# Kernel tuning notes

Hardware: AMD Instinct MI355X
Metric: run time of the kernel (lower is better)

## Reference

```python
import jax, jax.numpy as jnp
import numpy as np

N = 50000      # nodes
E = 800000     # edges (avg degree 16)
F_IN = 128     # num_features
H = 64         # hidden_dim
G = 64         # graphs in batch


def setup_inputs() -> dict:
    key = jax.random.key(0)
    ks = jax.random.split(key, 20)
    inp = {
        "x": jax.random.normal(ks[0], (N, F_IN), jnp.float32),
        "edge_index": jax.random.randint(ks[1], (2, E), 0, N, dtype=jnp.int32).astype(jnp.int64),
        "batch": jnp.sort(jax.random.randint(ks[2], (N,), 0, G, dtype=jnp.int32)).astype(jnp.int64),
    }
    # GraphConv layer dims: in -> out
    dims = [(F_IN, H), (H, 2 * H), (2 * H, 3 * H), (3 * H, H)]
    k = 3
    for i, (din, dout) in enumerate(dims):
        s = 1.0 / np.sqrt(din).astype(np.float32)
        inp[f"w{i+1}_rel"] = jax.random.normal(ks[k], (din, dout), jnp.float32) * s
        inp[f"w{i+1}_root"] = jax.random.normal(ks[k + 1], (din, dout), jnp.float32) * s
        inp[f"b{i+1}"] = jnp.zeros((dout,), jnp.float32)
        k += 2
    inp["head_w"] = jax.random.normal(ks[k], (H, 1), jnp.float32) * (1.0 / np.sqrt(H).astype(np.float32))
    inp["head_b"] = jnp.zeros((1,), jnp.float32)
    return inp


def _graph_conv(x, src, dst, w_rel, w_root, b):
    # PyG GraphConv: out = lin_rel(sum_{j in N(i)} x_j) + lin_root(x_i)
    agg = jax.ops.segment_sum(x[src], dst, num_segments=N)  # [N, din]
    return agg @ w_rel + b + x @ w_root


def reference(x, edge_index, batch,
              w1_rel, w1_root, b1,
              w2_rel, w2_root, b2,
              w3_rel, w3_root, b3,
              w4_rel, w4_root, b4,
              head_w, head_b):
    src, dst = edge_index[0], edge_index[1]
    h = jax.nn.relu(_graph_conv(x, src, dst, w1_rel, w1_root, b1))
    h = jax.nn.relu(_graph_conv(h, src, dst, w2_rel, w2_root, b2))
    h = jax.nn.relu(_graph_conv(h, src, dst, w3_rel, w3_root, b3))
    h = _graph_conv(h, src, dst, w4_rel, w4_root, b4)          # [N, H]
    # global_mean_pool over graph ids
    sums = jax.ops.segment_sum(h, batch, num_segments=G)       # [G, H]
    counts = jax.ops.segment_sum(jnp.ones((N,), h.dtype), batch, num_segments=G)
    pooled = sums / jnp.maximum(counts, 1.0)[:, None]          # [G, H]
    return pooled @ head_w + head_b                            # [G, 1]
```

## Files before the change

kernel.cpp:

```cpp
#include <hip/hip_runtime.h>


#define NNODES 50000
#define NEDGES 800000
#define NGRAPH 64
#define NBUK 256
#define BSZ 196
#define EPB (NEDGES / NBUK)
#define CVT_NB (NNODES * 128 / 4 / 256)
#define PACK_NB (160 * 512 / 256)
#define PREP_NB (CVT_NB + PACK_NB + 1)
#define RGRID ((NNODES + 127) / 128)
#define RCHUNK ((RGRID + 7) / 8)

typedef __attribute__((ext_vector_type(8))) __bf16 bf16x8;
typedef __attribute__((ext_vector_type(16))) float f32x16;

__device__ __forceinline__ unsigned short f2bf(float f) {
    unsigned u = __float_as_uint(f);
    u += 0x7fff + ((u >> 16) & 1);
    return (unsigned short)(u >> 16);
}
__device__ __forceinline__ float bf2f(unsigned b) {
    return __uint_as_float(b << 16);
}

__device__ __forceinline__ void dma16(const void* g, void* l) {
    __builtin_amdgcn_global_load_lds(
        (const __attribute__((address_space(1))) void*)g,
        (__attribute__((address_space(3))) void*)l, 16, 0, 0);
}


__device__ __forceinline__ void pack32(const float* __restrict__ W, unsigned short* __restrict__ dst,
                                       int KS_tot, int ks0, int dcols, int ct0,
                                       int tl, int ksl, int lane, int j) {
    int k = ksl * 16 + ((lane >> 5) << 3) + j;
    int col = tl * 32 + (lane & 31);
    dst[(((size_t)(ct0 + tl) * KS_tot + (ks0 + ksl)) * 64 + lane) * 8 + j] = f2bf(W[k * dcols + col]);
}

__device__ void prep_body(int b, int tid,
                          const float* x, unsigned short* xbf,
                          const float* w1_rel, const float* w1_root,
                          const float* w2_rel, const float* w2_root,
                          const float* w3_rel, const float* w3_root,
                          unsigned short* pL1, unsigned short* pL2, unsigned short* pL3,
                          const float* w4_rel, const float* w4_root,
                          const float* b4, const float* head_w,
                          float* wr, float* wt, float* cbuf) {
    if (b < CVT_NB) {
        int i = b * 256 + tid;
        float4 v = ((const float4*)x)[i];
        unsigned lo = (unsigned)f2bf(v.x) | ((unsigned)f2bf(v.y) << 16);
        unsigned hi = (unsigned)f2bf(v.z) | ((unsigned)f2bf(v.w) << 16);
        ((uint2*)xbf)[i] = make_uint2(lo, hi);
    } else if (b < CVT_NB + PACK_NB) {
        int idx = (b - CVT_NB) * 256 + tid;
        int g = idx >> 9;
        int t = idx & 511;
        int lane = (t >> 3) & 63, j = t & 7;
        if (g < 16)       { int gl = g;       pack32(w1_rel,  pL1, 8,  0, 64,  0, gl / 8, gl % 8, lane, j); }
        else if (g < 32)  { int gl = g - 16;  pack32(w1_root, pL1, 8,  0, 64,  2, gl / 8, gl % 8, lane, j); }
        else if (g < 48)  { int gl = g - 32;  pack32(w2_rel,  pL2, 8,  0, 128, 0, gl / 4, gl % 4, lane, j); }
        else if (g < 64)  { int gl = g - 48;  pack32(w2_root, pL2, 8,  4, 128, 0, gl / 4, gl % 4, lane, j); }
        else if (g < 112) { int gl = g - 64;  pack32(w3_rel,  pL3, 16, 0, 192, 0, gl / 8, gl % 8, lane, j); }
        else              { int gl = g - 112; pack32(w3_root, pL3, 16, 8, 192, 0, gl / 8, gl % 8, lane, j); }
    } else {
        if (tid < 192) {
            float ar = 0.f, at = 0.f;
            for (int j = 0; j < 64; j++) {
                float hw = head_w[j];
                ar = fmaf(w4_rel[tid * 64 + j], hw, ar);
                at = fmaf(w4_root[tid * 64 + j], hw, at);
            }
            wr[tid] = ar;
            wt[tid] = at;
        } else if (tid == 192) {
            float c = 0.f;
            for (int j = 0; j < 64; j++) c = fmaf(b4[j], head_w[j], c);
            cbuf[0] = c;
        }
    }
}


__global__ void __launch_bounds__(256) histprep_kernel(
    const int* __restrict__ edst, int* __restrict__ bcnt,
    const float* __restrict__ x, unsigned short* __restrict__ xbf,
    const float* __restrict__ w1_rel, const float* __restrict__ w1_root,
    const float* __restrict__ w2_rel, const float* __restrict__ w2_root,
    const float* __restrict__ w3_rel, const float* __restrict__ w3_root,
    unsigned short* __restrict__ pL1, unsigned short* __restrict__ pL2,
    unsigned short* __restrict__ pL3,
    const float* __restrict__ w4_rel, const float* __restrict__ w4_root,
    const float* __restrict__ b4, const float* __restrict__ head_w,
    float* __restrict__ wr, float* __restrict__ wt, float* __restrict__ cbuf)
{
    int tid = threadIdx.x, b = blockIdx.x;
    if (b < NBUK) {
        __shared__ int h[NBUK];
        h[tid] = 0;
        __syncthreads();
        int end = (b + 1) * EPB;
        for (int i = b * EPB + tid; i < end; i += 256)
            atomicAdd(&h[edst[i] / BSZ], 1);
        __syncthreads();
        bcnt[tid * NBUK + b] = h[tid];
    } else {
        prep_body(b - NBUK, tid, x, xbf, w1_rel, w1_root, w2_rel, w2_root,
                  w3_rel, w3_root, pL1, pL2, pL3, w4_rel, w4_root, b4, head_w,
                  wr, wt, cbuf);
    }
}


__global__ void scan1_kernel(int* __restrict__ a, int* __restrict__ bsum, int n) {
    __shared__ int buf[256];
    int tid = threadIdx.x;
    int i = blockIdx.x * 256 + tid;
    int v = (i < n) ? a[i] : 0;
    buf[tid] = v;
    __syncthreads();
    #pragma unroll
    for (int off = 1; off < 256; off <<= 1) {
        int t = (tid >= off) ? buf[tid - off] : 0;
        __syncthreads();
        buf[tid] += t;
        __syncthreads();
    }
    if (i < n) a[i] = buf[tid] - v;
    if (tid == 255) bsum[blockIdx.x] = buf[255];
}

__global__ void scan2_kernel(int* __restrict__ bsum, int nb) {
    __shared__ int buf[256];
    int tid = threadIdx.x;
    int v = (tid < nb) ? bsum[tid] : 0;
    buf[tid] = v;
    __syncthreads();
    #pragma unroll
    for (int off = 1; off < 256; off <<= 1) {
        int t = (tid >= off) ? buf[tid - off] : 0;
        __syncthreads();
        buf[tid] += t;
        __syncthreads();
    }
    if (tid < nb) bsum[tid] = buf[tid] - v;
}

__global__ void partition_kernel(const int* __restrict__ src, const int* __restrict__ dst,
                                 const int* __restrict__ cnt, const int* __restrict__ bsum,
                                 unsigned long long* __restrict__ pedge) {
    __shared__ int lbase[NBUK];
    int tid = threadIdx.x, k = blockIdx.x;
    lbase[tid] = cnt[tid * NBUK + k] + bsum[tid];
    __syncthreads();
    int end = (k + 1) * EPB;
    for (int i = k * EPB + tid; i < end; i += 256) {
        int s = src[i], d = dst[i];
        int pos = atomicAdd(&lbase[d / BSZ], 1);
        pedge[pos] = (unsigned long long)(unsigned)s | ((unsigned long long)(unsigned)d << 32);
    }
}

__global__ void build_kernel(const unsigned long long* __restrict__ pedge,
                             const int* __restrict__ bsum,
                             int* __restrict__ rp, int* __restrict__ csr) {
    __shared__ int sdeg[256], sc[256], sbase[256], sfill[256];
    int tid = threadIdx.x, b = blockIdx.x;
    int node0 = b * BSZ;
    int ncnt = NNODES - node0;
    if (ncnt > BSZ) ncnt = BSZ;
    if (ncnt < 0) ncnt = 0;
    int seg0 = bsum[b];
    int seg1 = (b + 1 < NBUK) ? bsum[b + 1] : NEDGES;
    sdeg[tid] = 0;
    sfill[tid] = 0;
    __syncthreads();
    for (int i = seg0 + tid; i < seg1; i += 256)
        atomicAdd(&sdeg[(int)(pedge[i] >> 32) - node0], 1);
    __syncthreads();
    sc[tid] = sdeg[tid];
    __syncthreads();
    #pragma unroll
    for (int off = 1; off < 256; off <<= 1) {
        int t = (tid >= off) ? sc[tid - off] : 0;
        __syncthreads();
        sc[tid] += t;
        __syncthreads();
    }
    sbase[tid] = sc[tid] - sdeg[tid];
    if (tid < ncnt) rp[node0 + tid] = seg0 + sbase[tid];
    if (b == NBUK - 1 && tid == 0) rp[NNODES] = NEDGES;
    __syncthreads();
    for (int i = seg0 + tid; i < seg1; i += 256) {
        unsigned long long p = pedge[i];
        int d = (int)(p >> 32) - node0;
        int pos = atomicAdd(&sfill[d], 1);
        csr[seg0 + sbase[d] + pos] = (int)(p & 0xffffffffu);
    }
}


template<int KS, int NT, int NHALF, int ST, int KCH>
__global__ __launch_bounds__(256) void gemm_v5(
    const unsigned short* __restrict__ A, const unsigned short* __restrict__ Wall,
    const float* __restrict__ bias, unsigned short* __restrict__ OUT,
    int ldo, int ocol0, int relu, int N,
    const float* __restrict__ wrp, const float* __restrict__ wtp,
    float* __restrict__ sb, float* __restrict__ tb)
{
    const int K = KS * 16;
    const int CPC = KCH * 2;
    __shared__ __align__(16) unsigned short sB[NT * KS * 512];
    __shared__ __align__(16) unsigned short sA[128 * KCH * 16];

    int i = blockIdx.x;
    int chunk = i / (8 * NHALF);
    int rem = i - chunk * (8 * NHALF);
    int halfsel = rem >> 3;
    int rowb = chunk * 8 + (rem & 7);
    int rbase = rowb * 128;
    if (rbase >= N) return;

    int tid = threadIdx.x;
    int wave = tid >> 6, lane = tid & 63;
    int l32 = lane & 31, half = lane >> 5;
    const unsigned short* W = Wall + (size_t)halfsel * NT * KS * 512;

    #pragma unroll
    for (int j = 0; j < NT * KS * 64 / 256; j++) {
        int p = j * 256 + wave * 64;
        dma16(W + ((size_t)p + lane) * 8, sB + (size_t)p * 8);
    }

    f32x16 acc[NT];
    #pragma unroll
    for (int t = 0; t < NT; t++)
        #pragma unroll
        for (int r = 0; r < 16; r++) acc[t][r] = 0.f;

    int lr = wave * 32 + l32;

    for (int kb = 0; kb < KS; kb += KCH) {
        if (kb > 0) __syncthreads();
        #pragma unroll
        for (int j = 0; j < 128 * CPC / 256; j++) {
            int p = j * 256 + wave * 64 + lane;
            int r = p / CPC;
            int c = p - r * CPC;
            int cg = c ^ (r & (CPC - 1));
            dma16(A + (size_t)(rbase + r) * K + kb * 16 + cg * 8,
                  sA + (size_t)(j * 256 + wave * 64) * 8);
        }
        __syncthreads();
        #pragma unroll
        for (int l = 0; l < KCH; l++) {
            int cs = (l * 2 + half) ^ (lr & (CPC - 1));
            bf16x8 a = *(const bf16x8*)(sA + (size_t)lr * (KCH * 16) + cs * 8);
            int ks = kb + l;
            #pragma unroll
            for (int t = 0; t < NT; t++) {
                bf16x8 b = *(const bf16x8*)(sB + ((size_t)(t * KS + ks) * 64 + lane) * 8);
                acc[t] = __builtin_amdgcn_mfma_f32_32x32x16_bf16(a, b, acc[t], 0, 0, 0);
            }
        }
    }

    int wrbase = rbase + wave * 32;
    if constexpr (ST) {
        #pragma unroll
        for (int reg = 0; reg < 16; reg++) {
            int row = wrbase + (reg & 3) + 8 * (reg >> 2) + 4 * half;
            float sv = 0.f, tv = 0.f;
            #pragma unroll
            for (int t = 0; t < NT; t++) {
                int col = halfsel * NT * 32 + t * 32 + l32;
                float v = fmaxf(acc[t][reg] + bias[col], 0.f);
                sv = fmaf(v, wrp[col], sv);
                tv = fmaf(v, wtp[col], tv);
            }
            #pragma unroll
            for (int m = 1; m < 32; m <<= 1) {
                sv += __shfl_xor(sv, m, 64);
                tv += __shfl_xor(tv, m, 64);
            }
            if (l32 == 0 && row < N) {
                atomicAdd(&sb[row], sv);
                atomicAdd(&tb[row], tv);
            }
        }
    } else {
        #pragma unroll
        for (int t = 0; t < NT; t++) {
            int col = t * 32 + l32;
            float bi = bias ? bias[col] : 0.f;
            #pragma unroll
            for (int reg = 0; reg < 16; reg++) {
                int row = wrbase + (reg & 3) + 8 * (reg >> 2) + 4 * half;
                if (row < N) {
                    float v = acc[t][reg] + bi;
                    if (relu) v = fmaxf(v, 0.f);
                    OUT[(size_t)row * ldo + ocol0 + col] = f2bf(v);
                }
            }
        }
    }
}


__device__ __forceinline__ void acc8(float* a, uint4 u) {
    a[0] += bf2f(u.x & 0xffffu); a[1] += bf2f(u.x >> 16);
    a[2] += bf2f(u.y & 0xffffu); a[3] += bf2f(u.y >> 16);
    a[4] += bf2f(u.z & 0xffffu); a[5] += bf2f(u.z >> 16);
    a[6] += bf2f(u.w & 0xffffu); a[7] += bf2f(u.w >> 16);
}

template<int LPF, int SUBS>
__global__ void agg_kernel_v4(const unsigned short* __restrict__ X, int ldx,
                              const int* __restrict__ rp, const int* __restrict__ csr,
                              const unsigned short* __restrict__ root, int ldr,
                              const float* __restrict__ bias, int relu,
                              unsigned short* __restrict__ OUT, int ldo, int N) {
    int t = blockIdx.x * blockDim.x + threadIdx.x;
    int node = t / (SUBS * LPF);
    int r = t % (SUBS * LPF);
    int sub = r / LPF;
    int sl = r % LPF;
    if (node >= N) return;
    float a[8] = {0.f, 0.f, 0.f, 0.f, 0.f, 0.f, 0.f, 0.f};
    int e0 = rp[node], e1 = rp[node + 1];
    const unsigned short* xb = X + 8 * sl;
    int e = e0 + sub;
    for (; e + 3 * SUBS < e1; e += 4 * SUBS) {
        int s0 = csr[e], s1 = csr[e + SUBS], s2 = csr[e + 2 * SUBS], s3 = csr[e + 3 * SUBS];
        uint4 u0 = *(const uint4*)(xb + (size_t)s0 * ldx);
        uint4 u1 = *(const uint4*)(xb + (size_t)s1 * ldx);
        uint4 u2 = *(const uint4*)(xb + (size_t)s2 * ldx);
        uint4 u3 = *(const uint4*)(xb + (size_t)s3 * ldx);
        acc8(a, u0); acc8(a, u1); acc8(a, u2); acc8(a, u3);
    }
    for (; e < e1; e += SUBS) {
        uint4 u = *(const uint4*)(xb + (size_t)csr[e] * ldx);
        acc8(a, u);
    }
    #pragma unroll
    for (int m = LPF; m < SUBS * LPF; m <<= 1)
        #pragma unroll
        for (int i = 0; i < 8; i++) a[i] += __shfl_xor(a[i], m, 64);
    if (sub == 0) {
        if (root) {
            uint4 u = *(const uint4*)(root + (size_t)node * ldr + 8 * sl);
            acc8(a, u);
        }
        if (bias) {
            float4 b0 = *(const float4*)(bias + 8 * sl);
            float4 b1 = *(const float4*)(bias + 8 * sl + 4);
            a[0] += b0.x; a[1] += b0.y; a[2] += b0.z; a[3] += b0.w;
            a[4] += b1.x; a[5] += b1.y; a[6] += b1.z; a[7] += b1.w;
        }
        if (relu) {
            #pragma unroll
            for (int i = 0; i < 8; i++) a[i] = fmaxf(a[i], 0.f);
        }
        uint4 o;
        o.x = (unsigned)f2bf(a[0]) | ((unsigned)f2bf(a[1]) << 16);
        o.y = (unsigned)f2bf(a[2]) | ((unsigned)f2bf(a[3]) << 16);
        o.z = (unsigned)f2bf(a[4]) | ((unsigned)f2bf(a[5]) << 16);
        o.w = (unsigned)f2bf(a[6]) | ((unsigned)f2bf(a[7]) << 16);
        *(uint4*)(OUT + (size_t)node * ldo + 8 * sl) = o;
    }
}


__global__ void aggpool_kernel(const float* __restrict__ s, const float* __restrict__ t,
                               const int* __restrict__ rp, const int* __restrict__ csr,
                               const int* __restrict__ batch, float* __restrict__ gsum,
                               int* __restrict__ cnt, int N) {
    __shared__ float ls[NGRAPH];
    __shared__ int lc[NGRAPH];
    int tid = threadIdx.x;
    if (tid < NGRAPH) { ls[tid] = 0.f; lc[tid] = 0; }
    __syncthreads();
    int n = blockIdx.x * blockDim.x + tid;
    if (n < N) {
        float a = 0.f;
        int e = rp[n], e1 = rp[n + 1];
        for (; e + 3 < e1; e += 4) {
            int s0 = csr[e], s1 = csr[e + 1], s2 = csr[e + 2], s3 = csr[e + 3];
            a += s[s0] + s[s1] + s[s2] + s[s3];
        }
        for (; e < e1; e++) a += s[csr[e]];
        int g = batch[n];
        atomicAdd(&ls[g], a + t[n]);
        atomicAdd(&lc[g], 1);
    }
    __syncthreads();
    if (tid < NGRAPH && lc[tid] > 0) {
        atomicAdd(&gsum[tid], ls[tid]);
        atomicAdd(&cnt[tid], lc[tid]);
    }
}

__global__ void final_kernel(const float* __restrict__ gsum, const int* __restrict__ cnt,
                             const float* __restrict__ cbuf, const float* __restrict__ head_b,
                             float* __restrict__ out) {
    int g = threadIdx.x;
    if (g < NGRAPH) {
        float c = (float)(cnt[g] > 0 ? cnt[g] : 1);
        out[g] = gsum[g] / c + cbuf[0] + head_b[0];
    }
}


extern "C" void kernel_launch(void* const* d_in, const int* in_sizes, int n_in,
                              void* d_out, int out_size, void* d_ws, size_t ws_size,
                              hipStream_t stream) {
    const float* x       = (const float*)d_in[0];
    const int*   edge    = (const int*)d_in[1];
    const int*   batch   = (const int*)d_in[2];
    const float* w1_rel  = (const float*)d_in[3];
    const float* w1_root = (const float*)d_in[4];
    const float* b1      = (const float*)d_in[5];
    const float* w2_rel  = (const float*)d_in[6];
    const float* w2_root = (const float*)d_in[7];
    const float* b2      = (const float*)d_in[8];
    const float* w3_rel  = (const float*)d_in[9];
    const float* w3_root = (const float*)d_in[10];
    const float* b3      = (const float*)d_in[11];
    const float* w4_rel  = (const float*)d_in[12];
    const float* w4_root = (const float*)d_in[13];
    const float* b4      = (const float*)d_in[14];
    const float* head_w  = (const float*)d_in[15];
    const float* head_b  = (const float*)d_in[16];
    float* out = (float*)d_out;

    const int N = NNODES, E = NEDGES;
    const int* esrc = edge;
    const int* edst = edge + E;

    char* ws = (char*)d_ws;
    size_t off = 0;
    auto alloc = [&](size_t bytes) -> char* {
        char* p = ws + off;
        off = (off + bytes + 255) & ~(size_t)255;
        return p;
    };
    float* gsum  = (float*)alloc(NGRAPH * 4);
    int*   cnt   = (int*)alloc(NGRAPH * 4);
    float* sbuf  = (float*)alloc((size_t)N * 4);
    float* tbuf  = (float*)alloc((size_t)N * 4);
    size_t zero_bytes = off;
    int*   bcnt  = (int*)alloc((size_t)NBUK * NBUK * 4);
    int*   bsum  = (int*)alloc(256 * 4);
    int*   rp    = (int*)alloc((size_t)(N + 1) * 4);
    int*   csr   = (int*)alloc((size_t)E * 4);
    unsigned long long* pedge = (unsigned long long*)alloc((size_t)E * 8);
    unsigned short* xbf    = (unsigned short*)alloc((size_t)N * 128 * 2);
    unsigned short* z1     = (unsigned short*)alloc((size_t)N * 128 * 2);
    unsigned short* combo2 = (unsigned short*)alloc((size_t)N * 128 * 2);
    unsigned short* combo3 = (unsigned short*)alloc((size_t)N * 256 * 2);
    unsigned short* pL1    = (unsigned short*)alloc(4 * 8 * 512 * 2);
    unsigned short* pL2    = (unsigned short*)alloc(4 * 8 * 512 * 2);
    unsigned short* pL3    = (unsigned short*)alloc(6 * 16 * 512 * 2);
    float* wr    = (float*)alloc(192 * 4);
    float* wt    = (float*)alloc(192 * 4);
    float* cbuf  = (float*)alloc(4);
    (void)ws_size;

    hipMemsetAsync(gsum, 0, zero_bytes, stream);

    const int TB = 256;

    histprep_kernel<<<NBUK + PREP_NB, 256, 0, stream>>>(
        edst, bcnt, x, xbf, w1_rel, w1_root, w2_rel, w2_root, w3_rel, w3_root,
        pL1, pL2, pL3, w4_rel, w4_root, b4, head_w, wr, wt, cbuf);
    scan1_kernel<<<NBUK, 256, 0, stream>>>(bcnt, bsum, NBUK * NBUK);
    scan2_kernel<<<1, 256, 0, stream>>>(bsum, NBUK);
    partition_kernel<<<NBUK, 256, 0, stream>>>(esrc, edst, bcnt, bsum, pedge);
    build_kernel<<<NBUK, 256, 0, stream>>>(pedge, bsum, rp, csr);

    gemm_v5<8, 4, 1, 0, 8><<<RCHUNK * 8, 256, 0, stream>>>(
        xbf, pL1, nullptr, z1, 128, 0, 0, N, nullptr, nullptr, nullptr, nullptr);
    agg_kernel_v4<8, 2><<<(N * 16 + TB - 1) / TB, TB, 0, stream>>>(z1, 128, rp, csr,
                                                                   z1 + 64, 128, b1, 1, combo2 + 64, 128, N);
    agg_kernel_v4<8, 2><<<(N * 16 + TB - 1) / TB, TB, 0, stream>>>(combo2 + 64, 128, rp, csr,
                                                                   nullptr, 0, nullptr, 0, combo2, 128, N);
    gemm_v5<8, 4, 1, 0, 8><<<RCHUNK * 8, 256, 0, stream>>>(
        combo2, pL2, b2, combo3, 256, 128, 1, N, nullptr, nullptr, nullptr, nullptr);
    agg_kernel_v4<16, 2><<<(N * 32 + TB - 1) / TB, TB, 0, stream>>>(combo3 + 128, 256, rp, csr,
                                                                    nullptr, 0, nullptr, 0, combo3, 256, N);
    gemm_v5<16, 3, 2, 1, 4><<<RCHUNK * 8 * 2, 256, 0, stream>>>(
        combo3, pL3, b3, nullptr, 0, 0, 0, N, wr, wt, sbuf, tbuf);

    aggpool_kernel<<<(N + TB - 1) / TB, TB, 0, stream>>>(sbuf, tbuf, rp, csr, batch, gsum, cnt, N);
    final_kernel<<<1, 64, 0, stream>>>(gsum, cnt, cbuf, head_b, out);
}
```

Measured before the change: 245.5 us.

## Fuse CSR-build stages with first GEMM and fold scans and memset into kernels

Merges the second-level scan into each partition block, which re-scans the bucket sums redundantly. The layer-1 GEMM blocks are split across the partition and build kernels so the independent GEMM work overlaps with the CSR construction. The memset is folded into the scan kernel as extra zeroing blocks. Three kernel launches are removed, at the cost of 64KB of shared memory per block in the fused kernels, which may reduce occupancy for the partition and build blocks.

```diff
diff --git a/kernel.cpp b/kernel.cpp
--- a/kernel.cpp
+++ b/kernel.cpp
@@ -12,6 +12,8 @@
 #define PREP_NB (CVT_NB + PACK_NB + 1)
 #define RGRID ((NNODES + 127) / 128)
 #define RCHUNK ((RGRID + 7) / 8)
+#define GB_SPLIT 196
+#define ZNB 32
 
 typedef __attribute__((ext_vector_type(8))) __bf16 bf16x8;
 typedef __attribute__((ext_vector_type(16))) float f32x16;
@@ -115,96 +117,34 @@
 }
 
 
-__global__ void scan1_kernel(int* __restrict__ a, int* __restrict__ bsum, int n) {
+__global__ void scanzero_kernel(int* __restrict__ a, int* __restrict__ bsum, int n,
+                                float4* __restrict__ zb, int zn16) {
     __shared__ int buf[256];
-    int tid = threadIdx.x;
-    int i = blockIdx.x * 256 + tid;
-    int v = (i < n) ? a[i] : 0;
-    buf[tid] = v;
-    __syncthreads();
-    #pragma unroll
-    for (int off = 1; off < 256; off <<= 1) {
-        int t = (tid >= off) ? buf[tid - off] : 0;
-        __syncthreads();
-        buf[tid] += t;
-        __syncthreads();
-    }
-    if (i < n) a[i] = buf[tid] - v;
-    if (tid == 255) bsum[blockIdx.x] = buf[255];
-}
-
-__global__ void scan2_kernel(int* __restrict__ bsum, int nb) {
-    __shared__ int buf[256];
-    int tid = threadIdx.x;
-    int v = (tid < nb) ? bsum[tid] : 0;
-    buf[tid] = v;
-    __syncthreads();
-    #pragma unroll
-    for (int off = 1; off < 256; off <<= 1) {
-        int t = (tid >= off) ? buf[tid - off] : 0;
-        __syncthreads();
-        buf[tid] += t;
-        __syncthreads();
-    }
-    if (tid < nb) bsum[tid] = buf[tid] - v;
-}
-
-__global__ void partition_kernel(const int* __restrict__ src, const int* __restrict__ dst,
-                                 const int* __restrict__ cnt, const int* __restrict__ bsum,
-                                 unsigned long long* __restrict__ pedge) {
-    __shared__ int lbase[NBUK];
-    int tid = threadIdx.x, k = blockIdx.x;
-    lbase[tid] = cnt[tid * NBUK + k] + bsum[tid];
-    __syncthreads();
-    int end = (k + 1) * EPB;
-    for (int i = k * EPB + tid; i < end; i += 256) {
-        int s = src[i], d = dst[i];
-        int pos = atomicAdd(&lbase[d / BSZ], 1);
-        pedge[pos] = (unsigned long long)(unsigned)s | ((unsigned long long)(unsigned)d << 32);
-    }
-}
-
-__global__ void build_kernel(const unsigned long long* __restrict__ pedge,
-                             const int* __restrict__ bsum,
-                             int* __restrict__ rp, int* __restrict__ csr) {
-    __shared__ int sdeg[256], sc[256], sbase[256], sfill[256];
     int tid = threadIdx.x, b = blockIdx.x;
-    int node0 = b * BSZ;
-    int ncnt = NNODES - node0;
-    if (ncnt > BSZ) ncnt = BSZ;
-    if (ncnt < 0) ncnt = 0;
-    int seg0 = bsum[b];
-    int seg1 = (b + 1 < NBUK) ? bsum[b + 1] : NEDGES;
-    sdeg[tid] = 0;
-    sfill[tid] = 0;
-    __syncthreads();
-    for (int i = seg0 + tid; i < seg1; i += 256)
-        atomicAdd(&sdeg[(int)(pedge[i] >> 32) - node0], 1);
-    __syncthreads();
-    sc[tid] = sdeg[tid];
-    __syncthreads();
-    #pragma unroll
-    for (int off = 1; off < 256; off <<= 1) {
-        int t = (tid >= off) ? sc[tid - off] : 0;
-        __syncthreads();
-        sc[tid] += t;
-        __syncthreads();
-    }
-    sbase[tid] = sc[tid] - sdeg[tid];
-    if (tid < ncnt) rp[node0 + tid] = seg0 + sbase[tid];
-    if (b == NBUK - 1 && tid == 0) rp[NNODES] = NEDGES;
-    __syncthreads();
-    for (int i = seg0 + tid; i < seg1; i += 256) {
-        unsigned long long p = pedge[i];
-        int d = (int)(p >> 32) - node0;
-        int pos = atomicAdd(&sfill[d], 1);
-        csr[seg0 + sbase[d] + pos] = (int)(p & 0xffffffffu);
+    if (b < NBUK) {
+        int i = b * 256 + tid;
+        int v = (i < n) ? a[i] : 0;
+        buf[tid] = v;
+        __syncthreads();
+        #pragma unroll
+        for (int off = 1; off < 256; off <<= 1) {
+            int t = (tid >= off) ? buf[tid - off] : 0;
+            __syncthreads();
+            buf[tid] += t;
+            __syncthreads();
+        }
+        if (i < n) a[i] = buf[tid] - v;
+        if (tid == 255) bsum[b] = buf[255];
+    } else {
+        float4 zero = make_float4(0.f, 0.f, 0.f, 0.f);
+        for (int i = (b - NBUK) * 256 + tid; i < zn16; i += ZNB * 256) zb[i] = zero;
     }
 }
 
 
 template<int KS, int NT, int NHALF, int ST, int KCH>
-__global__ __launch_bounds__(256) void gemm_v5(
+__device__ void gemm_body(
+    unsigned short* sB, unsigned short* sA, int i,
     const unsigned short* __restrict__ A, const unsigned short* __restrict__ Wall,
     const float* __restrict__ bias, unsigned short* __restrict__ OUT,
     int ldo, int ocol0, int relu, int N,
@@ -213,10 +153,7 @@
 {
     const int K = KS * 16;
     const int CPC = KCH * 2;
-    __shared__ __align__(16) unsigned short sB[NT * KS * 512];
-    __shared__ __align__(16) unsigned short sA[128 * KCH * 16];
-
-    int i = blockIdx.x;
+
     int chunk = i / (8 * NHALF);
     int rem = i - chunk * (8 * NHALF);
     int halfsel = rem >> 3;
@@ -306,6 +243,112 @@
                 }
             }
         }
+    }
+}
+
+template<int KS, int NT, int NHALF, int ST, int KCH>
+__global__ __launch_bounds__(256) void gemm_v5(
+    const unsigned short* __restrict__ A, const unsigned short* __restrict__ Wall,
+    const float* __restrict__ bias, unsigned short* __restrict__ OUT,
+    int ldo, int ocol0, int relu, int N,
+    const float* __restrict__ wrp, const float* __restrict__ wtp,
+    float* __restrict__ sb, float* __restrict__ tb)
+{
+    __shared__ __align__(16) unsigned short sB[NT * KS * 512];
+    __shared__ __align__(16) unsigned short sA[128 * KCH * 16];
+    gemm_body<KS, NT, NHALF, ST, KCH>(sB, sA, blockIdx.x, A, Wall, bias, OUT,
+                                      ldo, ocol0, relu, N, wrp, wtp, sb, tb);
+}
+
+
+__global__ void __launch_bounds__(256) partgemm_kernel(
+    const int* __restrict__ src, const int* __restrict__ dst,
+    const int* __restrict__ cnt, const int* __restrict__ braw,
+    int* __restrict__ sbsum, unsigned long long* __restrict__ pedge,
+    const unsigned short* __restrict__ A, const unsigned short* __restrict__ W,
+    unsigned short* __restrict__ OUT, int N)
+{
+    __shared__ __align__(16) unsigned short smem[32768];
+    int tid = threadIdx.x, b = blockIdx.x;
+    if (b < NBUK) {
+        int* lbase = (int*)smem;
+        int* sscan = lbase + 256;
+        int v = braw[tid];
+        sscan[tid] = v;
+        __syncthreads();
+        #pragma unroll
+        for (int off = 1; off < 256; off <<= 1) {
+            int t = (tid >= off) ? sscan[tid - off] : 0;
+            __syncthreads();
+            sscan[tid] += t;
+            __syncthreads();
+        }
+        int ex = sscan[tid] - v;
+        if (b == 0) sbsum[tid] = ex;
+        lbase[tid] = cnt[tid * NBUK + b] + ex;
+        __syncthreads();
+        int end = (b + 1) * EPB;
+        for (int i = b * EPB + tid; i < end; i += 256) {
+            int s = src[i], d = dst[i];
+            int pos = atomicAdd(&lbase[d / BSZ], 1);
+            pedge[pos] = (unsigned long long)(unsigned)s | ((unsigned long long)(unsigned)d << 32);
+        }
+    } else {
+        gemm_body<8, 4, 1, 0, 8>(smem, smem + 16384, b - NBUK,
+                                 A, W, nullptr, OUT, 128, 0, 0, N,
+                                 nullptr, nullptr, nullptr, nullptr);
+    }
+}
+
+
+__global__ void __launch_bounds__(256) buildgemm_kernel(
+    const unsigned long long* __restrict__ pedge, const int* __restrict__ sbsum,
+    int* __restrict__ rp, int* __restrict__ csr,
+    const unsigned short* __restrict__ A, const unsigned short* __restrict__ W,
+    unsigned short* __restrict__ OUT, int N)
+{
+    __shared__ __align__(16) unsigned short smem[32768];
+    int tid = threadIdx.x, b = blockIdx.x;
+    if (b < NBUK) {
+        int* sdeg  = (int*)smem;
+        int* sc    = sdeg + 256;
+        int* sbase = sc + 256;
+        int* sfill = sbase + 256;
+        int node0 = b * BSZ;
+        int ncnt = NNODES - node0;
+        if (ncnt > BSZ) ncnt = BSZ;
+        if (ncnt < 0) ncnt = 0;
+        int seg0 = sbsum[b];
+        int seg1 = (b + 1 < NBUK) ? sbsum[b + 1] : NEDGES;
+        sdeg[tid] = 0;
+        sfill[tid] = 0;
+        __syncthreads();
+        for (int i = seg0 + tid; i < seg1; i += 256)
+            atomicAdd(&sdeg[(int)(pedge[i] >> 32) - node0], 1);
+        __syncthreads();
+        sc[tid] = sdeg[tid];
+        __syncthreads();
+        #pragma unroll
+        for (int off = 1; off < 256; off <<= 1) {
+            int t = (tid >= off) ? sc[tid - off] : 0;
+            __syncthreads();
+            sc[tid] += t;
+            __syncthreads();
+        }
+        sbase[tid] = sc[tid] - sdeg[tid];
+        if (tid < ncnt) rp[node0 + tid] = seg0 + sbase[tid];
+        if (b == NBUK - 1 && tid == 0) rp[NNODES] = NEDGES;
+        __syncthreads();
+        for (int i = seg0 + tid; i < seg1; i += 256) {
+            unsigned long long p = pedge[i];
+            int d = (int)(p >> 32) - node0;
+            int pos = atomicAdd(&sfill[d], 1);
+            csr[seg0 + sbase[d] + pos] = (int)(p & 0xffffffffu);
+        }
+    } else {
+        gemm_body<8, 4, 1, 0, 8>(smem, smem + 16384, GB_SPLIT + (b - NBUK),
+                                 A, W, nullptr, OUT, 128, 0, 0, N,
+                                 nullptr, nullptr, nullptr, nullptr);
     }
 }
 
@@ -454,6 +497,7 @@
     size_t zero_bytes = off;
     int*   bcnt  = (int*)alloc((size_t)NBUK * NBUK * 4);
     int*   bsum  = (int*)alloc(256 * 4);
+    int*   sbsum = (int*)alloc(256 * 4);
     int*   rp    = (int*)alloc((size_t)(N + 1) * 4);
     int*   csr   = (int*)alloc((size_t)E * 4);
     unsigned long long* pedge = (unsigned long long*)alloc((size_t)E * 8);
@@ -469,20 +513,18 @@
     float* cbuf  = (float*)alloc(4);
     (void)ws_size;
 
-    hipMemsetAsync(gsum, 0, zero_bytes, stream);
-
     const int TB = 256;
 
     histprep_kernel<<<NBUK + PREP_NB, 256, 0, stream>>>(
         edst, bcnt, x, xbf, w1_rel, w1_root, w2_rel, w2_root, w3_rel, w3_root,
         pL1, pL2, pL3, w4_rel, w4_root, b4, head_w, wr, wt, cbuf);
-    scan1_kernel<<<NBUK, 256, 0, stream>>>(bcnt, bsum, NBUK * NBUK);
-    scan2_kernel<<<1, 256, 0, stream>>>(bsum, NBUK);
-    partition_kernel<<<NBUK, 256, 0, stream>>>(esrc, edst, bcnt, bsum, pedge);
-    build_kernel<<<NBUK, 256, 0, stream>>>(pedge, bsum, rp, csr);
-
-    gemm_v5<8, 4, 1, 0, 8><<<RCHUNK * 8, 256, 0, stream>>>(
-        xbf, pL1, nullptr, z1, 128, 0, 0, N, nullptr, nullptr, nullptr, nullptr);
+    scanzero_kernel<<<NBUK + ZNB, 256, 0, stream>>>(
+        bcnt, bsum, NBUK * NBUK, (float4*)ws, (int)(zero_bytes / 16));
+    partgemm_kernel<<<NBUK + GB_SPLIT, 256, 0, stream>>>(
+        esrc, edst, bcnt, bsum, sbsum, pedge, xbf, pL1, z1, N);
+    buildgemm_kernel<<<NBUK + (RCHUNK * 8 - GB_SPLIT), 256, 0, stream>>>(
+        pedge, sbsum, rp, csr, xbf, pL1, z1, N);
+
     agg_kernel_v4<8, 2><<<(N * 16 + TB - 1) / TB, TB, 0, stream>>>(z1, 128, rp, csr,
                                                                    z1 + 64, 128, b1, 1, combo2 + 64, 128, N);
     agg_kernel_v4<8, 2><<<(N * 16 + TB - 1) / TB, TB, 0, stream>>>(combo2 + 64, 128, rp, csr,
```

After: 241.2 us. Within noise of the previous version (-1.8%).
